# Kernel tuning notes

Hardware: AMD Instinct MI355X
Metric: run time of the kernel (lower is better)

The kernel has to match this reference:

```python
import jax, jax.numpy as jnp
import numpy as np

B, P, ENC, DEC, EMB, ATT, V, L = 32, 196, 2048, 512, 512, 512, 32000, 21
T = L - 1  # decode steps


def setup_inputs() -> dict:
    key = jax.random.key(0)
    ks = jax.random.split(key, 20)
    u = lambda k, s, a=0.1: jax.random.uniform(k, s, jnp.float32, -a, a)
    lens = jax.random.randint(ks[1], (B, 1), 5, L + 1)
    lens = lens.at[0, 0].set(L)  # force max_decode_len == T (static)
    return {
        'encoder_out': jax.random.normal(ks[0], (B, P, ENC), jnp.float32),
        'encoded_captions': jax.random.randint(ks[2], (B, L), 0, V),
        'caption_lengths': lens,
        'emb_W': u(ks[3], (V, EMB)),
        'W_ea': u(ks[4], (ATT, ENC), 0.02), 'b_ea': jnp.zeros((ATT,)),
        'W_da': u(ks[5], (ATT, DEC), 0.02), 'b_da': jnp.zeros((ATT,)),
        'w_fa': u(ks[6], (1, ATT), 0.02), 'b_fa': jnp.zeros((1,)),
        'W_ih': u(ks[7], (4 * DEC, EMB + ENC), 0.02), 'b_ih': jnp.zeros((4 * DEC,)),
        'W_hh': u(ks[8], (4 * DEC, DEC), 0.02), 'b_hh': jnp.zeros((4 * DEC,)),
        'W_h0': u(ks[9], (DEC, ENC), 0.02), 'b_h0': jnp.zeros((DEC,)),
        'W_c0': u(ks[10], (DEC, ENC), 0.02), 'b_c0': jnp.zeros((DEC,)),
        'W_fb': u(ks[11], (ENC, DEC), 0.02), 'b_fb': jnp.zeros((ENC,)),
        'W_fc': u(ks[12], (V, DEC)), 'b_fc': jnp.zeros((V,)),
    }


def reference(encoder_out, encoded_captions, caption_lengths, emb_W,
              W_ea, b_ea, W_da, b_da, w_fa, b_fa,
              W_ih, b_ih, W_hh, b_hh, W_h0, b_h0, W_c0, b_c0,
              W_fb, b_fb, W_fc, b_fc):
    # sort by caption length descending (as in torch forward)
    lens = caption_lengths[:, 0]
    sort_ind = jnp.argsort(-lens)
    lens_s = lens[sort_ind]
    enc = encoder_out[sort_ind]          # [B,P,ENC]
    caps = encoded_captions[sort_ind]    # [B,L]
    dec_lens = lens_s - 1

    mean_enc = enc.mean(axis=1)
    h0 = mean_enc @ W_h0.T + b_h0
    c0 = mean_enc @ W_c0.T + b_c0

    att1 = jnp.einsum('bpe,ae->bpa', enc, W_ea) + b_ea  # precompute encoder attn proj
    embs = emb_W[caps]                                   # [B,L,EMB]
    emb_seq = jnp.transpose(embs[:, :T], (1, 0, 2))      # [T,B,EMB] (teacher forcing)
    mask_seq = jnp.arange(T)[:, None] < dec_lens[None, :]  # [T,B]

    def step(carry, xs):
        h, c = carry
        emb_t, m = xs  # [B,EMB], [B] bool; m emulates shrinking batch_size_t
        att2 = h @ W_da.T + b_da
        e = jnp.maximum(att1 + att2[:, None, :], 0.0) @ w_fa[0] + b_fa[0]  # [B,P]
        alpha = jax.nn.softmax(e, axis=1)
        awe = jnp.einsum('bp,bpe->be', alpha, enc)
        gate = jax.nn.sigmoid(h @ W_fb.T + b_fb)
        x = jnp.concatenate([emb_t, gate * awe], axis=1)
        g = x @ W_ih.T + b_ih + h @ W_hh.T + b_hh
        i, f, gg, o = jnp.split(g, 4, axis=1)
        c_new = jax.nn.sigmoid(f) * c + jax.nn.sigmoid(i) * jnp.tanh(gg)
        h_new = jax.nn.sigmoid(o) * jnp.tanh(c_new)
        preds = h_new @ W_fc.T + b_fc  # dropout in eval mode (identity)
        mf = m[:, None]
        h = jnp.where(mf, h_new, h)
        c = jnp.where(mf, c_new, c)
        preds = preds * mf.astype(preds.dtype)
        alpha = alpha * mf.astype(alpha.dtype)
        return (h, c), (preds, alpha)

    _, (preds, alphas) = jax.lax.scan(step, (h0, c0), (emb_seq, mask_seq))
    predictions = jnp.transpose(preds, (1, 0, 2))  # [B,T,V]
    alphas = jnp.transpose(alphas, (1, 0, 2))      # [B,T,P]
    return predictions, alphas
```

## Files before the change

### kernel.cpp

```cpp
#include <hip/hip_runtime.h>
#include <hip/hip_bf16.h>
#include <cstddef>

#define NB 32
#define NP 196
#define NE 2048
#define ND 512
#define NV 32000
#define NL 21
#define NT 20

typedef __attribute__((ext_vector_type(8))) short short8;
typedef __attribute__((ext_vector_type(4))) float f32x4;

__device__ __forceinline__ unsigned short f2b(float f) {
    __hip_bfloat16 h = __float2bfloat16(f);
    return *reinterpret_cast<unsigned short*>(&h);
}
__device__ __forceinline__ float b2f_lo(unsigned int u) {
    union { unsigned int i; float f; } v; v.i = u << 16; return v.f;
}
__device__ __forceinline__ float b2f_hi(unsigned int u) {
    union { unsigned int i; float f; } v; v.i = u & 0xffff0000u; return v.f;
}


__global__ void k_sort(const int* __restrict__ lens, int* __restrict__ sind, int* __restrict__ dlens,
                       int* __restrict__ rowmap, int* __restrict__ mpad)
{
    int i = threadIdx.x;
    if (i < NB) {
        int li = lens[i];
        int r = 0;
        for (int j = 0; j < NB; ++j) {
            int lj = lens[j];
            if (lj > li || (lj == li && j < i)) ++r;
        }
        sind[r] = i;
        dlens[r] = li - 1;
    }
    __syncthreads();
    if (i == 0) {
        int c = 0;
        for (int t = 0; t < NT; ++t)
            for (int b = 0; b < NB; ++b)
                if (t < dlens[b]) rowmap[c++] = t * NB + b;
        int pad = (c + 63) & ~63;
        for (int r = c; r < pad; ++r) rowmap[r] = -1;
        mpad[0] = pad;
    }
}

__global__ __launch_bounds__(256) void k_mean(const float* __restrict__ enc, const int* __restrict__ sind,
                                              float* __restrict__ mean_enc)
{
    int b = blockIdx.y;
    int k = blockIdx.x * 256 + threadIdx.x;
    const float* e = enc + (size_t)sind[b] * NP * NE + k;
    float s0 = 0.f, s1 = 0.f, s2 = 0.f, s3 = 0.f;
    for (int p = 0; p < NP; p += 4) {
        s0 += e[(size_t)(p + 0) * NE];
        s1 += e[(size_t)(p + 1) * NE];
        s2 += e[(size_t)(p + 2) * NE];
        s3 += e[(size_t)(p + 3) * NE];
    }
    mean_enc[(size_t)b * NE + k] = (s0 + s1 + s2 + s3) * (1.0f / NP);
}

__global__ __launch_bounds__(256) void k_zero(const int* __restrict__ dlens, float* __restrict__ out)
{
    int b = blockIdx.x / NT, t = blockIdx.x % NT;
    if (t < dlens[b]) return;
    float4 z = {0.f, 0.f, 0.f, 0.f};
    float4* row = (float4*)(out + ((size_t)b * NT + t) * NV);
    for (int i = threadIdx.x; i < NV / 4; i += 256) row[i] = z;
}

__global__ __launch_bounds__(256) void gemm_skinny(
    const float* __restrict__ A0, const float* __restrict__ W0a, const float* __restrict__ W0b,
    const float* __restrict__ ba, const float* __restrict__ bb,
    float* __restrict__ C, float* __restrict__ xh)
{
    __shared__ float As[32][32];
    __shared__ float Ws[64][33];
    int n0 = blockIdx.x * 64;
    int tid = threadIdx.x;
    int lb = tid / 8, lkq = tid % 8;
    int b4 = (tid / 32) * 4, nl = (tid % 32) * 2;
    float acc[4][2] = {};
    for (int kt = 0; kt < NE; kt += 32) {
        float4 a4 = *reinterpret_cast<const float4*>(A0 + (size_t)lb * NE + kt + lkq * 4);
        As[lkq * 4 + 0][lb] = a4.x; As[lkq * 4 + 1][lb] = a4.y;
        As[lkq * 4 + 2][lb] = a4.z; As[lkq * 4 + 3][lb] = a4.w;
        #pragma unroll
        for (int r = 0; r < 2; ++r) {
            int s = tid + r * 256;
            int n_l = s / 8, kq = s % 8;
            int ng = n0 + n_l;
            const float* wrow = (ng < 512) ? (W0a + (size_t)ng * NE)
                                           : (W0b + (size_t)(ng - 512) * NE);
            float4 w4 = *reinterpret_cast<const float4*>(wrow + kt + kq * 4);
            Ws[n_l][kq * 4 + 0] = w4.x; Ws[n_l][kq * 4 + 1] = w4.y;
            Ws[n_l][kq * 4 + 2] = w4.z; Ws[n_l][kq * 4 + 3] = w4.w;
        }
        __syncthreads();
        #pragma unroll
        for (int k = 0; k < 32; ++k) {
            float4 av = *reinterpret_cast<const float4*>(&As[k][b4]);
            float w0 = Ws[nl][k], w1 = Ws[nl + 1][k];
            acc[0][0] += av.x * w0; acc[0][1] += av.x * w1;
            acc[1][0] += av.y * w0; acc[1][1] += av.y * w1;
            acc[2][0] += av.z * w0; acc[2][1] += av.z * w1;
            acc[3][0] += av.w * w0; acc[3][1] += av.w * w1;
        }
        __syncthreads();
    }
    #pragma unroll
    for (int j = 0; j < 2; ++j) {
        int ng = n0 + nl + j;
        float bias = (ng < 512) ? ba[ng] : bb[ng - 512];
        #pragma unroll
        for (int i = 0; i < 4; ++i) {
            float v = acc[i][j] + bias;
            int b = b4 + i;
            C[(size_t)b * 1024 + ng] = v;
            if (ng < 512) xh[(size_t)b * 3072 + 2560 + ng] = v;
        }
    }
}

__global__ __launch_bounds__(256) void gemm_att1_mfma(
    const float* __restrict__ enc, const float* __restrict__ W_ea,
    const float* __restrict__ bias, unsigned short* __restrict__ att1B,
    const int* __restrict__ sind)
{
    int fid = blockIdx.x;
    int c = fid & 7, x = (fid >> 3) & 7, pg = fid >> 6;
    int p = pg * 8 + c;
    if (p >= 98) return;
    int bm0 = p * 64, bn0 = x * 64;
    __shared__ unsigned short As[64][40];
    __shared__ unsigned short Bs[64][40];
    int tid = threadIdx.x;
    int w = tid >> 6, lane = tid & 63;
    int srow = tid >> 2, schunk = (tid & 3) * 8;
    int mg = bm0 + srow;
    int bidx = mg / NP, pp = mg - bidx * NP;
    const float* arow = enc + ((size_t)sind[bidx] * NP + pp) * NE + schunk;
    const float* brow = W_ea + (size_t)(bn0 + srow) * NE + schunk;
    int frow = lane & 15, fk = (lane >> 4) * 8;
    f32x4 acc[4] = {};
    for (int kt = 0; kt < NE; kt += 32) {
        float4 a0 = *reinterpret_cast<const float4*>(arow + kt);
        float4 a1 = *reinterpret_cast<const float4*>(arow + kt + 4);
        float4 b0 = *reinterpret_cast<const float4*>(brow + kt);
        float4 b1 = *reinterpret_cast<const float4*>(brow + kt + 4);
        uint4 av, bv;
        av.x = f2b(a0.x) | ((unsigned)f2b(a0.y) << 16);
        av.y = f2b(a0.z) | ((unsigned)f2b(a0.w) << 16);
        av.z = f2b(a1.x) | ((unsigned)f2b(a1.y) << 16);
        av.w = f2b(a1.z) | ((unsigned)f2b(a1.w) << 16);
        bv.x = f2b(b0.x) | ((unsigned)f2b(b0.y) << 16);
        bv.y = f2b(b0.z) | ((unsigned)f2b(b0.w) << 16);
        bv.z = f2b(b1.x) | ((unsigned)f2b(b1.y) << 16);
        bv.w = f2b(b1.z) | ((unsigned)f2b(b1.w) << 16);
        *reinterpret_cast<uint4*>(&As[srow][schunk]) = av;
        *reinterpret_cast<uint4*>(&Bs[srow][schunk]) = bv;
        __syncthreads();
        short8 af = *reinterpret_cast<const short8*>(&As[w * 16 + frow][fk]);
        #pragma unroll
        for (int n = 0; n < 4; ++n) {
            short8 bf = *reinterpret_cast<const short8*>(&Bs[n * 16 + frow][fk]);
            acc[n] = __builtin_amdgcn_mfma_f32_16x16x32_bf16(af, bf, acc[n], 0, 0, 0);
        }
        __syncthreads();
    }
    int crow = bm0 + w * 16 + (lane >> 4) * 4;
    int ccol0 = lane & 15;
    #pragma unroll
    for (int n = 0; n < 4; ++n) {
        int col = bn0 + n * 16 + ccol0;
        float bb2 = bias[col];
        #pragma unroll
        for (int i = 0; i < 4; ++i)
            att1B[(size_t)(crow + i) * ND + col] = f2b(acc[n][i] + bb2);
    }
}

__global__ __launch_bounds__(256) void gemm_preds_mfma(
    const unsigned short* __restrict__ hseqB, const float* __restrict__ W_fc,
    const float* __restrict__ bias, float* __restrict__ out,
    const int* __restrict__ rowmap, const int* __restrict__ mpad)
{
    int bm0 = blockIdx.x * 64;
    if (bm0 >= mpad[0]) return;
    int bn0 = blockIdx.y * 128;
    __shared__ unsigned short As[64][40];
    __shared__ unsigned short Bs[128][40];
    int tid = threadIdx.x;
    int w = tid >> 6, lane = tid & 63;
    int srow = tid >> 2, schunk = (tid & 3) * 8;
    int rid = rowmap[bm0 + srow];
    const unsigned short* aptr = hseqB + (size_t)(rid < 0 ? 0 : rid) * ND + schunk;
    const float* bptr0 = W_fc + (size_t)(bn0 + srow) * ND + schunk;
    const float* bptr1 = W_fc + (size_t)(bn0 + 64 + srow) * ND + schunk;
    int frow = lane & 15, fk = (lane >> 4) * 8;
    f32x4 acc[8] = {};
    for (int kt = 0; kt < ND; kt += 32) {
        uint4 av = *reinterpret_cast<const uint4*>(aptr + kt);
        float4 c0 = *reinterpret_cast<const float4*>(bptr0 + kt);
        float4 c1 = *reinterpret_cast<const float4*>(bptr0 + kt + 4);
        float4 d0 = *reinterpret_cast<const float4*>(bptr1 + kt);
        float4 d1 = *reinterpret_cast<const float4*>(bptr1 + kt + 4);
        uint4 bv0, bv1;
        bv0.x = f2b(c0.x) | ((unsigned)f2b(c0.y) << 16);
        bv0.y = f2b(c0.z) | ((unsigned)f2b(c0.w) << 16);
        bv0.z = f2b(c1.x) | ((unsigned)f2b(c1.y) << 16);
        bv0.w = f2b(c1.z) | ((unsigned)f2b(c1.w) << 16);
        bv1.x = f2b(d0.x) | ((unsigned)f2b(d0.y) << 16);
        bv1.y = f2b(d0.z) | ((unsigned)f2b(d0.w) << 16);
        bv1.z = f2b(d1.x) | ((unsigned)f2b(d1.y) << 16);
        bv1.w = f2b(d1.z) | ((unsigned)f2b(d1.w) << 16);
        *reinterpret_cast<uint4*>(&As[srow][schunk]) = av;
        *reinterpret_cast<uint4*>(&Bs[srow][schunk]) = bv0;
        *reinterpret_cast<uint4*>(&Bs[64 + srow][schunk]) = bv1;
        __syncthreads();
        short8 af = *reinterpret_cast<const short8*>(&As[w * 16 + frow][fk]);
        #pragma unroll
        for (int n = 0; n < 8; ++n) {
            short8 bf = *reinterpret_cast<const short8*>(&Bs[n * 16 + frow][fk]);
            acc[n] = __builtin_amdgcn_mfma_f32_16x16x32_bf16(af, bf, acc[n], 0, 0, 0);
        }
        __syncthreads();
    }
    int rl0 = w * 16 + (lane >> 4) * 4;
    int ccol0 = lane & 15;
    #pragma unroll
    for (int i = 0; i < 4; ++i) {
        int rm = rowmap[bm0 + rl0 + i];
        if (rm < 0) continue;
        int t = rm / NB, b = rm % NB;
        float* orow = out + ((size_t)b * NT + t) * NV;
        #pragma unroll
        for (int n = 0; n < 8; ++n) {
            int col = bn0 + n * 16 + ccol0;
            orow[col] = acc[n][i] + bias[col];
        }
    }
}

__global__ __launch_bounds__(256) void k_attg(
    const float* __restrict__ hc, const float* __restrict__ W_da, const float* __restrict__ W_fb,
    const float* __restrict__ b_da, const float* __restrict__ b_fb, float* __restrict__ attg)
{
    __shared__ float As[32][32];
    __shared__ float Ws[64][33];
    int n0 = blockIdx.x * 64;
    int tid = threadIdx.x;
    int lb = tid / 8, lkq = tid % 8;
    int b4 = (tid / 32) * 4, nl = (tid % 32) * 2;
    float acc[4][2] = {};
    for (int kt = 0; kt < 512; kt += 32) {
        float4 a4 = *reinterpret_cast<const float4*>(hc + (size_t)lb * 1024 + kt + lkq * 4);
        As[lkq * 4 + 0][lb] = a4.x; As[lkq * 4 + 1][lb] = a4.y;
        As[lkq * 4 + 2][lb] = a4.z; As[lkq * 4 + 3][lb] = a4.w;
        #pragma unroll
        for (int r = 0; r < 2; ++r) {
            int s = tid + r * 256;
            int n_l = s / 8, kq = s % 8;
            int ng = n0 + n_l;
            const float* wrow = (ng < 512) ? (W_da + (size_t)ng * 512)
                                           : (W_fb + (size_t)(ng - 512) * 512);
            float4 w4 = *reinterpret_cast<const float4*>(wrow + kt + kq * 4);
            Ws[n_l][kq * 4 + 0] = w4.x; Ws[n_l][kq * 4 + 1] = w4.y;
            Ws[n_l][kq * 4 + 2] = w4.z; Ws[n_l][kq * 4 + 3] = w4.w;
        }
        __syncthreads();
        #pragma unroll
        for (int k = 0; k < 32; ++k) {
            float4 av = *reinterpret_cast<const float4*>(&As[k][b4]);
            float w0 = Ws[nl][k], w1 = Ws[nl + 1][k];
            acc[0][0] += av.x * w0; acc[0][1] += av.x * w1;
            acc[1][0] += av.y * w0; acc[1][1] += av.y * w1;
            acc[2][0] += av.z * w0; acc[2][1] += av.z * w1;
            acc[3][0] += av.w * w0; acc[3][1] += av.w * w1;
        }
        __syncthreads();
    }
    #pragma unroll
    for (int j = 0; j < 2; ++j) {
        int ng = n0 + nl + j;
        float bias = (ng < 512) ? b_da[ng] : b_fb[ng - 512];
        #pragma unroll
        for (int i = 0; i < 4; ++i)
            attg[(size_t)(b4 + i) * 2560 + ng] = acc[i][j] + bias;
    }
}

__global__ __launch_bounds__(256) void k_e(
    const unsigned short* __restrict__ att1B, const float* __restrict__ attg,
    const float* __restrict__ w_fa, const float* __restrict__ b_fa,
    float* __restrict__ e)
{
    __shared__ float att2s[ND];
    __shared__ float wfas[ND];
    int b = blockIdx.y, tid = threadIdx.x;
    const float* ag = attg + (size_t)b * 2560;
    for (int d = tid; d < ND; d += 256) { att2s[d] = ag[d]; wfas[d] = w_fa[d]; }
    __syncthreads();
    int w = tid >> 6, lane = tid & 63;
    int p0 = blockIdx.x * 28;
    const unsigned short* a1 = att1B + ((size_t)b * NP + p0) * ND;
    #pragma unroll
    for (int i = 0; i < 7; ++i) {
        int p = w + 4 * i;
        const unsigned short* row = a1 + (size_t)p * ND;
        float s = 0.f;
        #pragma unroll
        for (int j = 0; j < 2; ++j) {
            int d = j * 256 + lane * 4;
            uint2 u = *reinterpret_cast<const uint2*>(row + d);
            float v0 = b2f_lo(u.x), v1 = b2f_hi(u.x);
            float v2 = b2f_lo(u.y), v3 = b2f_hi(u.y);
            float4 a2 = *reinterpret_cast<const float4*>(&att2s[d]);
            float4 wf = *reinterpret_cast<const float4*>(&wfas[d]);
            s += fmaxf(v0 + a2.x, 0.f) * wf.x + fmaxf(v1 + a2.y, 0.f) * wf.y
               + fmaxf(v2 + a2.z, 0.f) * wf.z + fmaxf(v3 + a2.w, 0.f) * wf.w;
        }
        for (int off = 32; off > 0; off >>= 1) s += __shfl_down(s, off);
        if (lane == 0) e[(size_t)b * NP + p0 + p] = s + b_fa[0];
    }
}

__global__ __launch_bounds__(256) void k_awe(
    const float* __restrict__ enc, const int* __restrict__ sind, const int* __restrict__ dlens,
    const int* __restrict__ caps, const float* __restrict__ emb_W,
    const float* __restrict__ e, const float* __restrict__ attg,
    float* __restrict__ xh, float* __restrict__ out_alpha, int t)
{
    __shared__ float es[256];
    __shared__ float red[256];
    int kc = blockIdx.x, b = blockIdx.y, tid = threadIdx.x;
    float ev = -1e30f;
    if (tid < NP) { float v = e[(size_t)b * NP + tid]; es[tid] = v; ev = v; }
    red[tid] = ev; __syncthreads();
    for (int s2 = 128; s2 > 0; s2 >>= 1) { if (tid < s2) red[tid] = fmaxf(red[tid], red[tid + s2]); __syncthreads(); }
    float m = red[0]; __syncthreads();
    float xe = (tid < NP) ? expf(es[tid] - m) : 0.f;
    red[tid] = xe; __syncthreads();
    for (int s2 = 128; s2 > 0; s2 >>= 1) { if (tid < s2) red[tid] += red[tid + s2]; __syncthreads(); }
    float inv = 1.0f / red[0];
    __syncthreads();
    es[tid] = xe * inv;
    __syncthreads();

    int k = kc * 256 + tid;
    const float* ec = enc + (size_t)sind[b] * NP * NE + k;
    float s0 = 0.f, s1 = 0.f, s2v = 0.f, s3 = 0.f;
    #pragma unroll 4
    for (int p = 0; p < NP; p += 4) {
        s0 += es[p + 0] * ec[(size_t)(p + 0) * NE];
        s1 += es[p + 1] * ec[(size_t)(p + 1) * NE];
        s2v += es[p + 2] * ec[(size_t)(p + 2) * NE];
        s3 += es[p + 3] * ec[(size_t)(p + 3) * NE];
    }
    float awe = (s0 + s1) + (s2v + s3);
    float gp = attg[(size_t)b * 2560 + 512 + k];
    float gate = 1.f / (1.f + expf(-gp));
    xh[(size_t)b * 3072 + 512 + k] = gate * awe;
    if (kc == 0) {
        bool live = (t < dlens[b]);
        if (tid < NP) out_alpha[((size_t)b * NT + t) * NP + tid] = live ? es[tid] : 0.f;
        const float* er = emb_W + (size_t)caps[sind[b] * NL + t] * ND;
        xh[(size_t)b * 3072 + tid] = er[tid];
        xh[(size_t)b * 3072 + 256 + tid] = er[256 + tid];
    }
}

__global__ __launch_bounds__(256) void k_gates(
    const float* __restrict__ xh, const float* __restrict__ W_ih, const float* __restrict__ W_hh,
    float* __restrict__ gpart)
{
    __shared__ float smem[3200];
    int blk = blockIdx.x, tid = threadIdx.x;
    int nt = blk & 31, ks = blk >> 5;
    float* As = smem;
    float (*Ws)[33] = (float(*)[33])(smem + 1024);
    int n0 = nt * 64;
    int lb = tid / 8, lkq = tid % 8;
    int b4 = (tid / 32) * 4, nl = (tid % 32) * 2;
    float acc[4][2] = {};
    for (int kt = ks * 768; kt < ks * 768 + 768; kt += 32) {
        float4 a4 = *reinterpret_cast<const float4*>(xh + (size_t)lb * 3072 + kt + lkq * 4);
        As[(lkq * 4 + 0) * 32 + lb] = a4.x; As[(lkq * 4 + 1) * 32 + lb] = a4.y;
        As[(lkq * 4 + 2) * 32 + lb] = a4.z; As[(lkq * 4 + 3) * 32 + lb] = a4.w;
        #pragma unroll
        for (int r = 0; r < 2; ++r) {
            int s = tid + r * 256;
            int n_l = s / 8, kq = s % 8;
            int ng = n0 + n_l;
            int kk = kt + kq * 4;
            const float* wrow = (kk < 2560) ? (W_ih + (size_t)ng * 2560 + kk)
                                            : (W_hh + (size_t)ng * 512 + (kk - 2560));
            float4 w4 = *reinterpret_cast<const float4*>(wrow);
            Ws[n_l][kq * 4 + 0] = w4.x; Ws[n_l][kq * 4 + 1] = w4.y;
            Ws[n_l][kq * 4 + 2] = w4.z; Ws[n_l][kq * 4 + 3] = w4.w;
        }
        __syncthreads();
        #pragma unroll
        for (int k = 0; k < 32; ++k) {
            float4 av = *reinterpret_cast<const float4*>(&As[k * 32 + b4]);
            float w0 = Ws[nl][k], w1 = Ws[nl + 1][k];
            acc[0][0] += av.x * w0; acc[0][1] += av.x * w1;
            acc[1][0] += av.y * w0; acc[1][1] += av.y * w1;
            acc[2][0] += av.z * w0; acc[2][1] += av.z * w1;
            acc[3][0] += av.w * w0; acc[3][1] += av.w * w1;
        }
        __syncthreads();
    }
    float* Cp = gpart + (size_t)ks * NB * 2048;
    #pragma unroll
    for (int j = 0; j < 2; ++j)
        #pragma unroll
        for (int i = 0; i < 4; ++i)
            Cp[(size_t)(b4 + i) * 2048 + n0 + nl + j] = acc[i][j];
}

__global__ __launch_bounds__(256) void k_cell(
    const float* __restrict__ gpart, const int* __restrict__ dlens,
    const float* __restrict__ b_ih, const float* __restrict__ b_hh,
    float* __restrict__ hc, unsigned short* __restrict__ hseqB, float* __restrict__ xh, int t)
{
    int b = blockIdx.x;
    for (int d = threadIdx.x; d < ND; d += 256) {
        float g0 = b_ih[d] + b_hh[d];
        float g1 = b_ih[512 + d] + b_hh[512 + d];
        float g2 = b_ih[1024 + d] + b_hh[1024 + d];
        float g3 = b_ih[1536 + d] + b_hh[1536 + d];
        #pragma unroll
        for (int ks = 0; ks < 4; ++ks) {
            const float* gp = gpart + ((size_t)ks * NB + b) * 2048;
            g0 += gp[d]; g1 += gp[512 + d]; g2 += gp[1024 + d]; g3 += gp[1536 + d];
        }
        float ig = 1.f / (1.f + expf(-g0));
        float fg = 1.f / (1.f + expf(-g1));
        float gt = tanhf(g2);
        float og = 1.f / (1.f + expf(-g3));
        float c_old = hc[(size_t)b * 1024 + 512 + d];
        float c_new = fg * c_old + ig * gt;
        float h_new = og * tanhf(c_new);
        hseqB[((size_t)t * NB + b) * ND + d] = f2b(h_new);
        if (t < dlens[b]) {
            hc[(size_t)b * 1024 + d] = h_new;
            hc[(size_t)b * 1024 + 512 + d] = c_new;
            xh[(size_t)b * 3072 + 2560 + d] = h_new;
        }
    }
}

extern "C" void kernel_launch(void* const* d_in, const int* in_sizes, int n_in,
                              void* d_out, int out_size, void* d_ws, size_t ws_size,
                              hipStream_t stream)
{
    const float* enc   = (const float*)d_in[0];
    const int*   caps  = (const int*)d_in[1];
    const int*   clens = (const int*)d_in[2];
    const float* emb_W = (const float*)d_in[3];
    const float* W_ea  = (const float*)d_in[4];
    const float* b_ea  = (const float*)d_in[5];
    const float* W_da  = (const float*)d_in[6];
    const float* b_da  = (const float*)d_in[7];
    const float* w_fa  = (const float*)d_in[8];
    const float* b_fa  = (const float*)d_in[9];
    const float* W_ih  = (const float*)d_in[10];
    const float* b_ih  = (const float*)d_in[11];
    const float* W_hh  = (const float*)d_in[12];
    const float* b_hh  = (const float*)d_in[13];
    const float* W_h0  = (const float*)d_in[14];
    const float* b_h0  = (const float*)d_in[15];
    const float* W_c0  = (const float*)d_in[16];
    const float* b_c0  = (const float*)d_in[17];
    const float* W_fb  = (const float*)d_in[18];
    const float* b_fb  = (const float*)d_in[19];
    const float* W_fc  = (const float*)d_in[20];
    const float* b_fc  = (const float*)d_in[21];

    float* out = (float*)d_out;
    float* out_alpha = out + (size_t)NB * NT * NV;

    int* iws    = (int*)d_ws;
    int* sind   = iws;
    int* dlens  = iws + 32;
    int* rowmap = iws + 64;
    int* mpad   = iws + 704;
    float* base = (float*)d_ws + 1024;
    float* mean_enc = base;
    float* hc    = mean_enc + NB * NE;
    float* attg  = hc + NB * 1024;
    float* xh    = attg + NB * 2560;
    float* e     = xh + NB * 3072;
    float* gpart = e + NB * NP;
    unsigned short* att1B = (unsigned short*)(gpart + 4 * NB * 2048);
    unsigned short* hseqB = att1B + (size_t)NB * NP * ND;

    k_sort<<<1, 64, 0, stream>>>(clens, sind, dlens, rowmap, mpad);
    k_zero<<<NB * NT, 256, 0, stream>>>(dlens, out);
    k_mean<<<dim3(NE / 256, NB), 256, 0, stream>>>(enc, sind, mean_enc);
    gemm_skinny<<<dim3(16), 256, 0, stream>>>(mean_enc, W_h0, W_c0, b_h0, b_c0, hc, xh);
    gemm_att1_mfma<<<dim3(832), 256, 0, stream>>>(enc, W_ea, b_ea, att1B, sind);

    for (int t = 0; t < NT; ++t) {
        k_attg<<<dim3(40), 256, 0, stream>>>(hc, W_da, W_fb, b_da, b_fb, attg);
        k_e<<<dim3(7, NB), 256, 0, stream>>>(att1B, attg, w_fa, b_fa, e);
        k_awe<<<dim3(8, NB), 256, 0, stream>>>(enc, sind, dlens, caps, emb_W,
                                               e, attg, xh, out_alpha, t);
        k_gates<<<dim3(128), 256, 0, stream>>>(xh, W_ih, W_hh, gpart);
        k_cell<<<dim3(NB), 256, 0, stream>>>(gpart, dlens, b_ih, b_hh, hc, hseqB, xh, t);
    }

    gemm_preds_mfma<<<dim3(10, NV / 128), 256, 0, stream>>>(hseqB, W_fc, b_fc, out, rowmap, mpad);
}
```

Before: 1.882 ms.

## Split-K the initial h0/c0 GEMM and remap preds GEMM block order

The skinny h0/c0 GEMM, which ran on only 16 blocks, is split along K into 8 slices writing partial sums into the gpart scratch buffer. A new small kernel reduces the slices and adds the biases. The preds GEMM moves to a 1D grid whose index mapping groups 8 column tiles (W_fc chunks) per XCD-style stride, for better L2 locality across chiplets. The cost is one extra kernel launch plus some guarded idle blocks in the padded grid.

```diff
diff --git a/kernel.cpp b/kernel.cpp
--- a/kernel.cpp
+++ b/kernel.cpp
@@ -76,19 +76,19 @@
     for (int i = threadIdx.x; i < NV / 4; i += 256) row[i] = z;
 }
 
-__global__ __launch_bounds__(256) void gemm_skinny(
+__global__ __launch_bounds__(256) void gemm_skinny_split(
     const float* __restrict__ A0, const float* __restrict__ W0a, const float* __restrict__ W0b,
-    const float* __restrict__ ba, const float* __restrict__ bb,
-    float* __restrict__ C, float* __restrict__ xh)
+    float* __restrict__ spart)
 {
     __shared__ float As[32][32];
     __shared__ float Ws[64][33];
     int n0 = blockIdx.x * 64;
+    int ks = blockIdx.y;
     int tid = threadIdx.x;
     int lb = tid / 8, lkq = tid % 8;
     int b4 = (tid / 32) * 4, nl = (tid % 32) * 2;
     float acc[4][2] = {};
-    for (int kt = 0; kt < NE; kt += 32) {
+    for (int kt = ks * 256; kt < ks * 256 + 256; kt += 32) {
         float4 a4 = *reinterpret_cast<const float4*>(A0 + (size_t)lb * NE + kt + lkq * 4);
         As[lkq * 4 + 0][lb] = a4.x; As[lkq * 4 + 1][lb] = a4.y;
         As[lkq * 4 + 2][lb] = a4.z; As[lkq * 4 + 3][lb] = a4.w;
@@ -115,17 +115,26 @@
         }
         __syncthreads();
     }
+    float* Cp = spart + (size_t)ks * NB * 1024;
     #pragma unroll
-    for (int j = 0; j < 2; ++j) {
-        int ng = n0 + nl + j;
-        float bias = (ng < 512) ? ba[ng] : bb[ng - 512];
-        #pragma unroll
-        for (int i = 0; i < 4; ++i) {
-            float v = acc[i][j] + bias;
-            int b = b4 + i;
-            C[(size_t)b * 1024 + ng] = v;
-            if (ng < 512) xh[(size_t)b * 3072 + 2560 + ng] = v;
-        }
+    for (int j = 0; j < 2; ++j)
+        #pragma unroll
+        for (int i = 0; i < 4; ++i)
+            Cp[(size_t)(b4 + i) * 1024 + n0 + nl + j] = acc[i][j];
+}
+
+__global__ __launch_bounds__(256) void k_hc0(
+    const float* __restrict__ spart, const float* __restrict__ ba, const float* __restrict__ bb,
+    float* __restrict__ hc, float* __restrict__ xh)
+{
+    int b = blockIdx.x;
+    for (int ng = threadIdx.x; ng < 1024; ng += 256) {
+        float s = (ng < 512) ? ba[ng] : bb[ng - 512];
+        #pragma unroll
+        for (int ks = 0; ks < 8; ++ks)
+            s += spart[(size_t)ks * NB * 1024 + (size_t)b * 1024 + ng];
+        hc[(size_t)b * 1024 + ng] = s;
+        if (ng < 512) xh[(size_t)b * 3072 + 2560 + ng] = s;
     }
 }
 
@@ -192,9 +201,15 @@
     const float* __restrict__ bias, float* __restrict__ out,
     const int* __restrict__ rowmap, const int* __restrict__ mpad)
 {
-    int bm0 = blockIdx.x * 64;
+    int fid = blockIdx.x;
+    int c = fid & 7;
+    int rem = fid >> 3;
+    int m = rem % 10, g = rem / 10;
+    int n = g * 8 + c;
+    if (n >= 250) return;
+    int bm0 = m * 64;
     if (bm0 >= mpad[0]) return;
-    int bn0 = blockIdx.y * 128;
+    int bn0 = n * 128;
     __shared__ unsigned short As[64][40];
     __shared__ unsigned short Bs[128][40];
     int tid = threadIdx.x;
@@ -227,9 +242,9 @@
         __syncthreads();
         short8 af = *reinterpret_cast<const short8*>(&As[w * 16 + frow][fk]);
         #pragma unroll
-        for (int n = 0; n < 8; ++n) {
-            short8 bf = *reinterpret_cast<const short8*>(&Bs[n * 16 + frow][fk]);
-            acc[n] = __builtin_amdgcn_mfma_f32_16x16x32_bf16(af, bf, acc[n], 0, 0, 0);
+        for (int nn = 0; nn < 8; ++nn) {
+            short8 bf = *reinterpret_cast<const short8*>(&Bs[nn * 16 + frow][fk]);
+            acc[nn] = __builtin_amdgcn_mfma_f32_16x16x32_bf16(af, bf, acc[nn], 0, 0, 0);
         }
         __syncthreads();
     }
@@ -242,9 +257,9 @@
         int t = rm / NB, b = rm % NB;
         float* orow = out + ((size_t)b * NT + t) * NV;
         #pragma unroll
-        for (int n = 0; n < 8; ++n) {
-            int col = bn0 + n * 16 + ccol0;
-            orow[col] = acc[n][i] + bias[col];
+        for (int nn = 0; nn < 8; ++nn) {
+            int col = bn0 + nn * 16 + ccol0;
+            orow[col] = acc[nn][i] + bias[col];
         }
     }
 }
@@ -506,7 +521,8 @@
     k_sort<<<1, 64, 0, stream>>>(clens, sind, dlens, rowmap, mpad);
     k_zero<<<NB * NT, 256, 0, stream>>>(dlens, out);
     k_mean<<<dim3(NE / 256, NB), 256, 0, stream>>>(enc, sind, mean_enc);
-    gemm_skinny<<<dim3(16), 256, 0, stream>>>(mean_enc, W_h0, W_c0, b_h0, b_c0, hc, xh);
+    gemm_skinny_split<<<dim3(16, 8), 256, 0, stream>>>(mean_enc, W_h0, W_c0, gpart);
+    k_hc0<<<dim3(NB), 256, 0, stream>>>(gpart, b_h0, b_c0, hc, xh);
     gemm_att1_mfma<<<dim3(832), 256, 0, stream>>>(enc, W_ea, b_ea, att1B, sind);
 
     for (int t = 0; t < NT; ++t) {
@@ -518,5 +534,5 @@
         k_cell<<<dim3(NB), 256, 0, stream>>>(gpart, dlens, b_ih, b_hh, hc, hseqB, xh, t);
     }
 
-    gemm_preds_mfma<<<dim3(10, NV / 128), 256, 0, stream>>>(hseqB, W_fc, b_fc, out, rowmap, mpad);
-}
+    gemm_preds_mfma<<<dim3(2560), 256, 0, stream>>>(hseqB, W_fc, b_fc, out, rowmap, mpad);
+}
```

New measurement: 1.778 ms. -5.6%, faster.
